# Kernel optimization log

Hardware: AMD Instinct MI355X
Metric: run time of the kernel (lower is better)

Reference implementation:

```python
import jax, jax.numpy as jnp
import numpy as np

HEADS = 16
EPS = 1e-5

def _ln(x, g, b):
    m = jnp.mean(x, axis=-1, keepdims=True)
    v = jnp.mean((x - m) ** 2, axis=-1, keepdims=True)
    return (x - m) * jax.lax.rsqrt(v + EPS) * g + b

def setup_inputs() -> dict:
    key = jax.random.key(0)
    ks = jax.random.split(key, 12)
    B, N, C, H = 4, 2048, 1024, 4096
    d = {}
    d['x'] = jax.random.normal(ks[0], (B, N, C), jnp.float32)
    d['pos_embed'] = jax.random.normal(ks[1], (1, N, C), jnp.float32)
    # LayerNorm params (normq, normk, normv, norm)
    for nm in ['nq', 'nk', 'nv', 'n']:
        d[nm + '_g'] = jnp.ones((C,), jnp.float32)
        d[nm + '_b'] = jnp.zeros((C,), jnp.float32)
    s = 1.0 / np.sqrt(C)
    d['wq'] = jax.random.uniform(ks[2], (C, C), jnp.float32, -s, s)
    d['bq'] = jnp.zeros((C,), jnp.float32)
    d['wk'] = jax.random.uniform(ks[3], (C, C), jnp.float32, -s, s)
    d['bk'] = jnp.zeros((C,), jnp.float32)
    d['wv'] = jax.random.uniform(ks[4], (C, C), jnp.float32, -s, s)
    d['bv'] = jnp.zeros((C,), jnp.float32)
    d['wp'] = jax.random.uniform(ks[5], (C, C), jnp.float32, -s, s)
    d['bp'] = jnp.zeros((C,), jnp.float32)
    d['w1'] = jax.random.uniform(ks[6], (C, H), jnp.float32, -s, s)
    d['b1'] = jnp.zeros((H,), jnp.float32)
    sh = 1.0 / np.sqrt(H)
    d['w2'] = jax.random.uniform(ks[7], (H, C), jnp.float32, -sh, sh)
    d['b2'] = jnp.zeros((C,), jnp.float32)
    return d

def reference(x, pos_embed, nq_g, nq_b, nk_g, nk_b, nv_g, nv_b, wq, bq, wk, bk, wv, bv, wp, bp, n_g, n_b, w1, b1, w2, b2):
    B, N, C = x.shape
    hd = C // HEADS
    scale = hd ** -0.5
    q_in = x
    k_in = x + pos_embed
    v_in = x + pos_embed
    # Attention (eval mode: dropout = identity)
    q = (_ln(q_in, nq_g, nq_b) @ wq + bq).reshape(B, N, HEADS, hd)
    k = (_ln(k_in, nk_g, nk_b) @ wk + bk).reshape(B, N, HEADS, hd)
    v = (_ln(v_in, nv_g, nv_b) @ wv + bv).reshape(B, N, HEADS, hd)
    attn = jnp.einsum('bqhd,bkhd->bhqk', q, k) * scale
    attn = jax.nn.softmax(attn, axis=-1)
    out = jnp.einsum('bhqk,bkhd->bqhd', attn, v).reshape(B, N, C)
    out = out @ wp + bp
    # residual + MLP
    h = q_in + out
    y = _ln(h, n_g, n_b) @ w1 + b1
    y = jnp.where(y >= 0, y, 0.1 * y)  # LeakyReLU(0.1)
    y = y @ w2 + b2
    return h + y
```

## Files before the change

kernel.cpp:

```cpp
#include <hip/hip_runtime.h>
#include <hip/hip_bf16.h>

#define DEV __device__ __forceinline__

typedef __attribute__((ext_vector_type(8))) short short8;
typedef __attribute__((ext_vector_type(4))) short short4v;
typedef __attribute__((ext_vector_type(4))) float f32x4;
typedef __attribute__((ext_vector_type(2))) int int2v;

constexpr int Bb   = 4;
constexpr int SEQ  = 2048;
constexpr int C    = 1024;
constexpr int HID  = 4096;
constexpr int NH   = 16;
constexpr int HD   = 64;
constexpr int MTOT = Bb * SEQ;

DEV unsigned bfbits(float f) {
  unsigned x = __float_as_uint(f);
  return (x + 0x7fffu + ((x >> 16) & 1u)) >> 16;
}

DEV short f2bf(float f) { return (short)bfbits(f); }

DEV unsigned packrn(float a, float b) {
  unsigned ua = __float_as_uint(a) + 0x8000u;
  unsigned ub = __float_as_uint(b) + 0x8000u;
  return __builtin_amdgcn_perm(ub, ua, 0x07060302u);
}

DEV float fexp2(float x) {
#if __has_builtin(__builtin_amdgcn_exp2f)
  return __builtin_amdgcn_exp2f(x);
#else
  float r;
  asm("v_exp_f32 %0, %1" : "=v"(r) : "v"(x));
  return r;
#endif
}

DEV void gload16(const void* g, void* l) {
  __builtin_amdgcn_global_load_lds((const __attribute__((address_space(1))) void*)g,
                                   (__attribute__((address_space(3))) void*)l, 16, 0, 0);
}

DEV f32x4 mfma16(short4v a, short4v b, f32x4 c) {
#if __has_builtin(__builtin_amdgcn_mfma_f32_16x16x16bf16_1k)
  return __builtin_amdgcn_mfma_f32_16x16x16bf16_1k(a, b, c, 0, 0, 0);
#else
  asm volatile("v_mfma_f32_16x16x16_bf16 %0, %1, %2, %0" : "+v"(c) : "v"(a), "v"(b));
  return c;
#endif
}

DEV void transpose_body(const float* __restrict__ src, short* __restrict__ dst,
                        int R, int Cc) {
  __shared__ float t[32][33];
  int tx = threadIdx.x & 31, ty = threadIdx.x >> 5;
  int c0 = blockIdx.x * 32, r0 = blockIdx.y * 32;
  #pragma unroll
  for (int i = 0; i < 4; i++)
    t[ty + i * 8][tx] = src[(size_t)(r0 + ty + i * 8) * Cc + c0 + tx];
  __syncthreads();
  #pragma unroll
  for (int i = 0; i < 4; i++)
    dst[(size_t)(c0 + ty + i * 8) * R + r0 + tx] = f2bf(t[tx][ty + i * 8]);
}

__global__ void k_transpose_w(const float* __restrict__ src, short* __restrict__ dst,
                              int R, int Cc) {
  transpose_body(src, dst, R, Cc);
}

__global__ void k_transpose_w4(const float* __restrict__ s0, const float* __restrict__ s1,
                               const float* __restrict__ s2, const float* __restrict__ s3,
                               short* __restrict__ d0, short* __restrict__ d1,
                               short* __restrict__ d2, short* __restrict__ d3) {
  const float* s = blockIdx.z == 0 ? s0 : blockIdx.z == 1 ? s1 : blockIdx.z == 2 ? s2 : s3;
  short*       d = blockIdx.z == 0 ? d0 : blockIdx.z == 1 ? d1 : blockIdx.z == 2 ? d2 : d3;
  transpose_body(s, d, C, C);
}

__global__ void k_transpose_v(const short* __restrict__ V, short* __restrict__ Vt) {
  __shared__ short t[32][33];
  int tx = threadIdx.x & 31, ty = threadIdx.x >> 5;
  int plane = blockIdx.z;
  int b = plane >> 4, h = plane & 15;
  int n0 = blockIdx.x * 32, d0 = blockIdx.y * 32;
  #pragma unroll
  for (int i = 0; i < 4; i++)
    t[ty + i * 8][tx] = V[(size_t)(b * SEQ + n0 + ty + i * 8) * C + h * HD + d0 + tx];
  __syncthreads();
  #pragma unroll
  for (int i = 0; i < 4; i++)
    Vt[((size_t)plane * HD + d0 + ty + i * 8) * SEQ + n0 + tx] = t[tx][ty + i * 8];
}

__global__ void k_ln_qkv(const float* __restrict__ x, const float* __restrict__ pos,
                         const float* __restrict__ nqg, const float* __restrict__ nqb,
                         const float* __restrict__ nkg, const float* __restrict__ nkb,
                         const float* __restrict__ nvg, const float* __restrict__ nvb,
                         short* __restrict__ xq, short* __restrict__ xk,
                         short* __restrict__ xv) {
  int row = blockIdx.x, tid = threadIdx.x;
  int n = row & (SEQ - 1);
  float a4[4], p4[4];
  float s1 = 0, s2 = 0, t1 = 0, t2 = 0;
  #pragma unroll
  for (int i = 0; i < 4; i++) {
    int c = tid + i * 256;
    float a = x[(size_t)row * C + c];
    float p = pos[(size_t)n * C + c] + a;
    a4[i] = a; p4[i] = p;
    s1 += a; s2 += a * a; t1 += p; t2 += p * p;
  }
  #pragma unroll
  for (int off = 32; off; off >>= 1) {
    s1 += __shfl_xor(s1, off, 64);
    s2 += __shfl_xor(s2, off, 64);
    t1 += __shfl_xor(t1, off, 64);
    t2 += __shfl_xor(t2, off, 64);
  }
  __shared__ float red[4][4];
  int wave = tid >> 6, lane = tid & 63;
  if (lane == 0) { red[wave][0] = s1; red[wave][1] = s2; red[wave][2] = t1; red[wave][3] = t2; }
  __syncthreads();
  s1 = red[0][0] + red[1][0] + red[2][0] + red[3][0];
  s2 = red[0][1] + red[1][1] + red[2][1] + red[3][1];
  t1 = red[0][2] + red[1][2] + red[2][2] + red[3][2];
  t2 = red[0][3] + red[1][3] + red[2][3] + red[3][3];
  float mq = s1 * (1.f / C), mk = t1 * (1.f / C);
  float rq = rsqrtf(s2 * (1.f / C) - mq * mq + 1e-5f);
  float rk = rsqrtf(t2 * (1.f / C) - mk * mk + 1e-5f);
  #pragma unroll
  for (int i = 0; i < 4; i++) {
    int c = tid + i * 256;
    float nq_ = (a4[i] - mq) * rq;
    float nk_ = (p4[i] - mk) * rk;
    xq[(size_t)row * C + c] = f2bf(nq_ * nqg[c] + nqb[c]);
    xk[(size_t)row * C + c] = f2bf(nk_ * nkg[c] + nkb[c]);
    xv[(size_t)row * C + c] = f2bf(nk_ * nvg[c] + nvb[c]);
  }
}

__global__ void k_ln1(const float* __restrict__ h, const float* __restrict__ g,
                      const float* __restrict__ bta, short* __restrict__ out) {
  int row = blockIdx.x, tid = threadIdx.x;
  float a4[4];
  float s1 = 0, s2 = 0;
  #pragma unroll
  for (int i = 0; i < 4; i++) {
    int c = tid + i * 256;
    float a = h[(size_t)row * C + c];
    a4[i] = a; s1 += a; s2 += a * a;
  }
  #pragma unroll
  for (int off = 32; off; off >>= 1) {
    s1 += __shfl_xor(s1, off, 64);
    s2 += __shfl_xor(s2, off, 64);
  }
  __shared__ float red[4][2];
  int wave = tid >> 6, lane = tid & 63;
  if (lane == 0) { red[wave][0] = s1; red[wave][1] = s2; }
  __syncthreads();
  s1 = red[0][0] + red[1][0] + red[2][0] + red[3][0];
  s2 = red[0][1] + red[1][1] + red[2][1] + red[3][1];
  float m = s1 * (1.f / C);
  float r = rsqrtf(s2 * (1.f / C) - m * m + 1e-5f);
  #pragma unroll
  for (int i = 0; i < 4; i++) {
    int c = tid + i * 256;
    out[(size_t)row * C + c] = f2bf((a4[i] - m) * r * g[c] + bta[c]);
  }
}

template <int MODE>
DEV void gemm8_body(const short* __restrict__ A, const short* __restrict__ Bt,
                    const float* __restrict__ bias, const float* __restrict__ resid,
                    void* __restrict__ outp, int Nn, int Kk, float scale,
                    int m0, int n0, short* __restrict__ sA, short* __restrict__ sB) {
  constexpr int AO = 128 * 64, BO = 256 * 64;
  const int tid = threadIdx.x;
  const int wave = tid >> 6, lane = tid & 63, quad = lane >> 4, l15 = lane & 15;
  const int wm = (wave >> 2) * 64, wn = (wave & 3) * 64;

  const int sr = tid >> 3, su = tid & 7;
  const int sx = (su ^ (sr & 7)) * 8;
  const short* gA0 = A + (size_t)(m0 + sr) * Kk + sx;
  const short* gA1 = gA0 + (size_t)64 * Kk;
  const short* gB0 = Bt + (size_t)(n0 + sr) * Kk + sx;
  const short* gB1 = gB0 + (size_t)64 * Kk;
  const short* gB2 = gB0 + (size_t)128 * Kk;
  const short* gB3 = gB0 + (size_t)192 * Kk;

  const f32x4 fzero = {0.f, 0.f, 0.f, 0.f};
  f32x4 acc[4][4];
  #pragma unroll
  for (int mi = 0; mi < 4; mi++)
    #pragma unroll
    for (int ni = 0; ni < 4; ni++) acc[mi][ni] = fzero;

  const int nkt = Kk >> 6;

  auto stg = [&](int t) {
    const int b_ = t % 3, ko = t << 6;
    gload16(gA0 + ko, &sA[(size_t)b_ * AO + (size_t)tid * 8]);
    gload16(gA1 + ko, &sA[(size_t)b_ * AO + (size_t)(512 + tid) * 8]);
    gload16(gB0 + ko, &sB[(size_t)b_ * BO + (size_t)tid * 8]);
    gload16(gB1 + ko, &sB[(size_t)b_ * BO + (size_t)(512 + tid) * 8]);
    gload16(gB2 + ko, &sB[(size_t)b_ * BO + (size_t)(1024 + tid) * 8]);
    gload16(gB3 + ko, &sB[(size_t)b_ * BO + (size_t)(1536 + tid) * 8]);
  };
  auto stgA_ = [&](int t) {
    const int b_ = t % 3, ko = t << 6;
    gload16(gA0 + ko, &sA[(size_t)b_ * AO + (size_t)tid * 8]);
    gload16(gA1 + ko, &sA[(size_t)b_ * AO + (size_t)(512 + tid) * 8]);
    gload16(gB0 + ko, &sB[(size_t)b_ * BO + (size_t)tid * 8]);
  };
  auto stgB_ = [&](int t) {
    const int b_ = t % 3, ko = t << 6;
    gload16(gB1 + ko, &sB[(size_t)b_ * BO + (size_t)(512 + tid) * 8]);
    gload16(gB2 + ko, &sB[(size_t)b_ * BO + (size_t)(1024 + tid) * 8]);
    gload16(gB3 + ko, &sB[(size_t)b_ * BO + (size_t)(1536 + tid) * 8]);
  };

  stg(0);
  if (nkt > 1) stg(1);

  for (int t = 0; t < nkt; t++) {
    if (t + 1 < nkt) asm volatile("s_waitcnt vmcnt(6)" ::: "memory");
    else             asm volatile("s_waitcnt vmcnt(0)" ::: "memory");
    __builtin_amdgcn_s_barrier();
    const short* a_ = &sA[(size_t)(t % 3) * AO];
    const short* b_ = &sB[(size_t)(t % 3) * BO];
    short8 av[4][2];
    {
      short8 bv[2][2];
      #pragma unroll
      for (int m2 = 0; m2 < 4; m2++) {
        const int rA = wm + m2 * 16 + l15, sw = rA & 7;
        #pragma unroll
        for (int ks = 0; ks < 2; ks++)
          av[m2][ks] = *(const short8*)&a_[rA * 64 + ((ks * 4 + quad) ^ sw) * 8];
      }
      #pragma unroll
      for (int n2 = 0; n2 < 2; n2++) {
        const int rB = wn + n2 * 16 + l15, sw = rB & 7;
        #pragma unroll
        for (int ks = 0; ks < 2; ks++)
          bv[n2][ks] = *(const short8*)&b_[rB * 64 + ((ks * 4 + quad) ^ sw) * 8];
      }
      if (t + 2 < nkt) stgA_(t + 2);
      __builtin_amdgcn_s_barrier();
      asm volatile("s_waitcnt lgkmcnt(0)" ::: "memory");
      __builtin_amdgcn_sched_barrier(0);
      __builtin_amdgcn_s_setprio(1);
      #pragma unroll
      for (int ks = 0; ks < 2; ks++)
        #pragma unroll
        for (int m2 = 0; m2 < 4; m2++)
          #pragma unroll
          for (int n2 = 0; n2 < 2; n2++)
            acc[m2][n2] = __builtin_amdgcn_mfma_f32_16x16x32_bf16(
                av[m2][ks], bv[n2][ks], acc[m2][n2], 0, 0, 0);
      __builtin_amdgcn_s_setprio(0);
      __builtin_amdgcn_s_barrier();
    }
    {
      short8 bv[2][2];
      #pragma unroll
      for (int n2 = 0; n2 < 2; n2++) {
        const int rB = wn + (2 + n2) * 16 + l15, sw = rB & 7;
        #pragma unroll
        for (int ks = 0; ks < 2; ks++)
          bv[n2][ks] = *(const short8*)&b_[rB * 64 + ((ks * 4 + quad) ^ sw) * 8];
      }
      if (t + 2 < nkt) stgB_(t + 2);
      __builtin_amdgcn_s_barrier();
      asm volatile("s_waitcnt lgkmcnt(0)" ::: "memory");
      __builtin_amdgcn_sched_barrier(0);
      __builtin_amdgcn_s_setprio(1);
      #pragma unroll
      for (int ks = 0; ks < 2; ks++)
        #pragma unroll
        for (int m2 = 0; m2 < 4; m2++)
          #pragma unroll
          for (int n2 = 0; n2 < 2; n2++)
            acc[m2][2 + n2] = __builtin_amdgcn_mfma_f32_16x16x32_bf16(
                av[m2][ks], bv[n2][ks], acc[m2][2 + n2], 0, 0, 0);
      __builtin_amdgcn_s_setprio(0);
      __builtin_amdgcn_s_barrier();
    }
  }

  float bb[4];
  #pragma unroll
  for (int ni = 0; ni < 4; ni++) bb[ni] = bias[n0 + wn + ni * 16 + l15];
  #pragma unroll
  for (int mi = 0; mi < 4; mi++) {
    #pragma unroll
    for (int ni = 0; ni < 4; ni++) {
      #pragma unroll
      for (int r = 0; r < 4; r++) {
        int row = m0 + wm + mi * 16 + quad * 4 + r;
        int col = n0 + wn + ni * 16 + l15;
        float v = (acc[mi][ni][r] + bb[ni]) * scale;
        if constexpr (MODE == 1) v = v >= 0.f ? v : 0.1f * v;
        if constexpr (MODE == 2)
          ((float*)outp)[(size_t)row * Nn + col] = resid[(size_t)row * Nn + col] + v;
        else
          ((short*)outp)[(size_t)row * Nn + col] = f2bf(v);
      }
    }
  }
}

template <int MODE>
__global__ __launch_bounds__(512, 1)
void k_gemm8(const short* __restrict__ A, const short* __restrict__ Bt,
             const float* __restrict__ bias, const float* __restrict__ resid,
             void* __restrict__ outp, int Nn, int Kk) {
  __shared__ __align__(16) short sA[3 * 128 * 64];
  __shared__ __align__(16) short sB[3 * 256 * 64];
  gemm8_body<MODE>(A, Bt, bias, resid, outp, Nn, Kk, 1.0f,
                   blockIdx.x * 128, blockIdx.y * 256, sA, sB);
}

template <int MODE>
DEV void gemm2_body(const short* __restrict__ A, const short* __restrict__ Bt,
                    const float* __restrict__ bias, const float* __restrict__ resid,
                    void* __restrict__ outp, int Nn, int Kk, float scale,
                    int m0, int n0, short* __restrict__ sA, short* __restrict__ sB) {
  constexpr int TO = 256 * 64;
  const int tid = threadIdx.x;
  const int wave = tid >> 6, lane = tid & 63, quad = lane >> 4, l15 = lane & 15;
  const int wm = (wave >> 2) * 128, wn = (wave & 3) * 64;

  const int sr = tid >> 3, su = tid & 7;
  const int sx = (su ^ (sr & 7)) * 8;
  const short* gA0 = A + (size_t)(m0 + sr) * Kk + sx;
  const short* gB0 = Bt + (size_t)(n0 + sr) * Kk + sx;

  const f32x4 fzero = {0.f, 0.f, 0.f, 0.f};
  f32x4 acc[8][4];
  #pragma unroll
  for (int mi = 0; mi < 8; mi++)
    #pragma unroll
    for (int ni = 0; ni < 4; ni++) acc[mi][ni] = fzero;

  const int nkt = Kk >> 6;

  auto stgPair = [&](int t, int p) {
    const int b_ = t & 1, ko = t << 6;
    gload16(gA0 + (size_t)(p * 64) * Kk + ko,
            &sA[(size_t)b_ * TO + (size_t)p * 4096 + (size_t)tid * 8]);
    gload16(gB0 + (size_t)(p * 64) * Kk + ko,
            &sB[(size_t)b_ * TO + (size_t)p * 4096 + (size_t)tid * 8]);
  };

  #pragma unroll
  for (int p = 0; p < 4; p++) stgPair(0, p);

  for (int t = 0; t < nkt; t++) {
    asm volatile("s_waitcnt vmcnt(0)" ::: "memory");
    __builtin_amdgcn_s_barrier();
    const short* a_ = &sA[(size_t)(t & 1) * TO];
    const short* b_ = &sB[(size_t)(t & 1) * TO];
    short8 bv[4][2];
    #pragma unroll
    for (int ph = 0; ph < 4; ph++) {
      short8 av[2][2];
      #pragma unroll
      for (int m2 = 0; m2 < 2; m2++) {
        const int rA = wm + (ph * 2 + m2) * 16 + l15, sw = rA & 7;
        #pragma unroll
        for (int ks = 0; ks < 2; ks++)
          av[m2][ks] = *(const short8*)&a_[rA * 64 + ((ks * 4 + quad) ^ sw) * 8];
      }
      if (ph == 0) {
        #pragma unroll
        for (int n2 = 0; n2 < 4; n2++) {
          const int rB = wn + n2 * 16 + l15, sw = rB & 7;
          #pragma unroll
          for (int ks = 0; ks < 2; ks++)
            bv[n2][ks] = *(const short8*)&b_[rB * 64 + ((ks * 4 + quad) ^ sw) * 8];
        }
      }
      if (t + 1 < nkt) stgPair(t + 1, ph);
      __builtin_amdgcn_s_barrier();
      asm volatile("s_waitcnt lgkmcnt(0)" ::: "memory");
      __builtin_amdgcn_sched_barrier(0);
      __builtin_amdgcn_s_setprio(1);
      #pragma unroll
      for (int ks = 0; ks < 2; ks++)
        #pragma unroll
        for (int m2 = 0; m2 < 2; m2++)
          #pragma unroll
          for (int n2 = 0; n2 < 4; n2++)
            acc[ph * 2 + m2][n2] = __builtin_amdgcn_mfma_f32_16x16x32_bf16(
                av[m2][ks], bv[n2][ks], acc[ph * 2 + m2][n2], 0, 0, 0);
      __builtin_amdgcn_s_setprio(0);
      __builtin_amdgcn_s_barrier();
    }
  }

  float bb[4];
  #pragma unroll
  for (int ni = 0; ni < 4; ni++) bb[ni] = bias[n0 + wn + ni * 16 + l15];
  #pragma unroll
  for (int mi = 0; mi < 8; mi++) {
    #pragma unroll
    for (int ni = 0; ni < 4; ni++) {
      #pragma unroll
      for (int r = 0; r < 4; r++) {
        int row = m0 + wm + mi * 16 + quad * 4 + r;
        int col = n0 + wn + ni * 16 + l15;
        float v = (acc[mi][ni][r] + bb[ni]) * scale;
        if constexpr (MODE == 1) v = v >= 0.f ? v : 0.1f * v;
        if constexpr (MODE == 2)
          ((float*)outp)[(size_t)row * Nn + col] = resid[(size_t)row * Nn + col] + v;
        else
          ((short*)outp)[(size_t)row * Nn + col] = f2bf(v);
      }
    }
  }
}

template <int MODE>
__global__ __launch_bounds__(512, 1)
void k_gemm2(const short* __restrict__ A, const short* __restrict__ Bt,
             const float* __restrict__ bias, const float* __restrict__ resid,
             void* __restrict__ outp, int Nn, int Kk) {
  __shared__ __align__(16) short sA[2 * 256 * 64];
  __shared__ __align__(16) short sB[2 * 256 * 64];
  gemm2_body<MODE>(A, Bt, bias, resid, outp, Nn, Kk, 1.0f,
                   blockIdx.x * 256, blockIdx.y * 256, sA, sB);
}

__global__ __launch_bounds__(512, 1)
void k_gemm2_qkv(const short* __restrict__ xq, const short* __restrict__ xk,
                 const short* __restrict__ xv,
                 const short* __restrict__ wqT, const short* __restrict__ wkT,
                 const short* __restrict__ wvT,
                 const float* __restrict__ bq, const float* __restrict__ bk,
                 const float* __restrict__ bv,
                 short* __restrict__ Qm, short* __restrict__ Km, short* __restrict__ Vm) {
  __shared__ __align__(16) short sA[2 * 256 * 64];
  __shared__ __align__(16) short sB[2 * 256 * 64];
  const int z = blockIdx.z;
  const short* A    = z == 0 ? xq : z == 1 ? xk : xv;
  const short* Bt   = z == 0 ? wqT : z == 1 ? wkT : wvT;
  const float* bias = z == 0 ? bq : z == 1 ? bk : bv;
  short* outp       = z == 0 ? Qm : z == 1 ? Km : Vm;
  const float scale = z == 0 ? 0.1803368801111244f : 1.0f;
  gemm2_body<0>(A, Bt, bias, nullptr, outp, C, C, scale,
                blockIdx.x * 256, blockIdx.y * 256, sA, sB);
}

__global__ __launch_bounds__(256, 4)
void k_attn(const short* __restrict__ Q, const short* __restrict__ K,
            const short* __restrict__ Vt, short* __restrict__ O) {
  __shared__ __align__(16) short sK[2][64 * 64];
  __shared__ __align__(16) short sV[2][64 * 64];
  const int tid = threadIdx.x;
  const int bh = blockIdx.x;
  const int b = bh >> 4, h = bh & 15;
  const int q0 = blockIdx.y * 128;
  const int wave = tid >> 6, lane = tid & 63, quad = lane >> 4, l15 = lane & 15;
  const int wm = wave * 32;
  const size_t tokBase = (size_t)b * SEQ;

  short8 qf[2][2];
  #pragma unroll
  for (int qi = 0; qi < 2; qi++)
    #pragma unroll
    for (int hf = 0; hf < 2; hf++)
      qf[qi][hf] = *(const short8*)(Q + (tokBase + q0 + wm + qi * 16 + l15) * C
                                    + h * HD + hf * 32 + quad * 8);

  const int r0 = tid >> 3,        c0s = ((tid & 7) ^ (r0 & 7)) * 8;
  const int r1 = (tid + 256) >> 3, c1s = ((tid & 7) ^ (r1 & 7)) * 8;
  const short* gK0 = K + (tokBase + r0) * C + h * HD + c0s;
  const short* gK1 = K + (tokBase + r1) * C + h * HD + c1s;
  const short* gV0 = Vt + ((size_t)bh * HD + r0) * SEQ + c0s;
  const short* gV1 = Vt + ((size_t)bh * HD + r1) * SEQ + c1s;
  short* lK0 = &sK[0][tid * 8];
  short* lK1 = &sK[0][(tid + 256) * 8];
  short* lV0 = &sV[0][tid * 8];
  short* lV1 = &sV[0][(tid + 256) * 8];
  constexpr int BUFO = 64 * 64;

#define STAGE(bufsel, kb) {                                   \
    int kk = (kb) * 64, bo = (bufsel) * BUFO;                 \
    gload16(gK0 + (size_t)kk * C, lK0 + bo);                  \
    gload16(gK1 + (size_t)kk * C, lK1 + bo);                  \
    gload16(gV0 + kk,             lV0 + bo);                  \
    gload16(gV1 + kk,             lV1 + bo); }

  const f32x4 fzero = {0.f, 0.f, 0.f, 0.f};
  const short4v onesv = {0x3F80, 0x3F80, 0x3F80, 0x3F80};
  f32x4 o[2][4];
  f32x4 oSum[2] = {fzero, fzero};
  #pragma unroll
  for (int qi = 0; qi < 2; qi++)
    #pragma unroll
    for (int di = 0; di < 4; di++) o[qi][di] = fzero;

  const int sw = l15 & 7;

  STAGE(0, 0)

  for (int kb = 0; kb < SEQ / 64; kb++) {
    const int buf = kb & 1;
    __syncthreads();
    if (kb + 1 < SEQ / 64) STAGE(buf ^ 1, kb + 1)

    unsigned pk[4][2][2];
    #pragma unroll
    for (int ki = 0; ki < 4; ki++) {
      const int krow = (ki * 16 + l15) * 64;
      short8 a0 = *(const short8*)&sK[buf][krow + ((0 + quad) ^ sw) * 8];
      short8 a1 = *(const short8*)&sK[buf][krow + ((4 + quad) ^ sw) * 8];
      #pragma unroll
      for (int qi = 0; qi < 2; qi++) {
        f32x4 st = __builtin_amdgcn_mfma_f32_16x16x32_bf16(a0, qf[qi][0], fzero, 0, 0, 0);
        st = __builtin_amdgcn_mfma_f32_16x16x32_bf16(a1, qf[qi][1], st, 0, 0, 0);
        float p0 = fexp2(st[0]), p1 = fexp2(st[1]);
        float p2 = fexp2(st[2]), p3 = fexp2(st[3]);
        pk[ki][qi][0] = packrn(p0, p1);
        pk[ki][qi][1] = packrn(p2, p3);
      }
    }

    #pragma unroll
    for (int ki = 0; ki < 4; ki++) {
      short4v bv[4];
      const int g = ((ki * 2 + (quad >> 1)) ^ sw) * 8 + (quad & 1) * 4;
      #pragma unroll
      for (int di = 0; di < 4; di++)
        bv[di] = *(const short4v*)&sV[buf][(di * 16 + l15) * 64 + g];
      #pragma unroll
      for (int qi = 0; qi < 2; qi++) {
        int2v t; t.x = (int)pk[ki][qi][0]; t.y = (int)pk[ki][qi][1];
        short4v aP = __builtin_bit_cast(short4v, t);
        oSum[qi] = mfma16(aP, onesv, oSum[qi]);
        #pragma unroll
        for (int di = 0; di < 4; di++)
          o[qi][di] = mfma16(aP, bv[di], o[qi][di]);
      }
    }
  }
#undef STAGE

  float linv[2][4];
  #pragma unroll
  for (int qi = 0; qi < 2; qi++)
    #pragma unroll
    for (int r = 0; r < 4; r++)
      linv[qi][r] = 1.0f / oSum[qi][r];

  #pragma unroll
  for (int qi = 0; qi < 2; qi++)
    #pragma unroll
    for (int di = 0; di < 4; di++)
      #pragma unroll
      for (int r = 0; r < 4; r++) {
        int row = q0 + wm + qi * 16 + quad * 4 + r;
        int col = h * HD + di * 16 + l15;
        O[(tokBase + row) * C + col] = f2bf(o[qi][di][r] * linv[qi][r]);
      }
}

extern "C" void kernel_launch(void* const* d_in, const int* in_sizes, int n_in,
                              void* d_out, int out_size, void* d_ws, size_t ws_size,
                              hipStream_t stream) {
  const float* x   = (const float*)d_in[0];
  const float* pos = (const float*)d_in[1];
  const float* nqg = (const float*)d_in[2];
  const float* nqb = (const float*)d_in[3];
  const float* nkg = (const float*)d_in[4];
  const float* nkb = (const float*)d_in[5];
  const float* nvg = (const float*)d_in[6];
  const float* nvb = (const float*)d_in[7];
  const float* ng  = (const float*)d_in[8];
  const float* nb  = (const float*)d_in[9];
  const float* wq  = (const float*)d_in[10];
  const float* bq  = (const float*)d_in[11];
  const float* wk  = (const float*)d_in[12];
  const float* bk  = (const float*)d_in[13];
  const float* wv  = (const float*)d_in[14];
  const float* bv  = (const float*)d_in[15];
  const float* wp  = (const float*)d_in[16];
  const float* bp  = (const float*)d_in[17];
  const float* w1  = (const float*)d_in[18];
  const float* b1  = (const float*)d_in[19];
  const float* w2  = (const float*)d_in[20];
  const float* b2  = (const float*)d_in[21];

  char* ws = (char*)d_ws;
  const size_t MB = 1u << 20;
  short* wqT  = (short*)(ws + 0 * MB);
  short* wkT  = (short*)(ws + 2 * MB);
  short* wvT  = (short*)(ws + 4 * MB);
  short* wpT  = (short*)(ws + 6 * MB);
  short* w1T  = (short*)(ws + 8 * MB);
  short* w2T  = (short*)(ws + 16 * MB);
  short* xq   = (short*)(ws + 24 * MB);
  short* xk   = (short*)(ws + 40 * MB);
  short* xv   = (short*)(ws + 56 * MB);
  short* Qm   = (short*)(ws + 72 * MB);
  short* Km   = (short*)(ws + 88 * MB);
  short* Vm   = (short*)(ws + 104 * MB);
  short* Vt   = (short*)(ws + 120 * MB);
  short* y1   = (short*)(ws + 72 * MB);
  short* Ob   = xk;
  short* hln  = xq;
  float* hbuf = (float*)(ws + 136 * MB);
  (void)ws_size; (void)in_sizes; (void)n_in; (void)out_size;

  dim3 blk(256);
  k_transpose_w4<<<dim3(32, 32, 4), blk, 0, stream>>>(wq, wk, wv, wp, wqT, wkT, wvT, wpT);
  k_transpose_w<<<dim3(128, 32), blk, 0, stream>>>(w1, w1T, C, HID);
  k_transpose_w<<<dim3(32, 128), blk, 0, stream>>>(w2, w2T, HID, C);
  k_ln_qkv<<<dim3(MTOT), blk, 0, stream>>>(x, pos, nqg, nqb, nkg, nkb, nvg, nvb, xq, xk, xv);
  k_gemm2_qkv<<<dim3(MTOT / 256, C / 256, 3), dim3(512), 0, stream>>>(
      xq, xk, xv, wqT, wkT, wvT, bq, bk, bv, Qm, Km, Vm);
  k_transpose_v<<<dim3(SEQ / 32, HD / 32, Bb * NH), blk, 0, stream>>>(Vm, Vt);
  k_attn<<<dim3(Bb * NH, SEQ / 128), blk, 0, stream>>>(Qm, Km, Vt, Ob);
  k_gemm8<2><<<dim3(MTOT / 128, C / 256), dim3(512), 0, stream>>>(Ob, wpT, bp, x, hbuf, C, C);
  k_ln1<<<dim3(MTOT), blk, 0, stream>>>(hbuf, ng, nb, hln);
  k_gemm2<1><<<dim3(MTOT / 256, HID / 256), dim3(512), 0, stream>>>(hln, w1T, b1, nullptr,
                                                                    y1, HID, C);
  k_gemm8<2><<<dim3(MTOT / 128, C / 256), dim3(512), 0, stream>>>(y1, w2T, b2, hbuf,
                                                                  (float*)d_out, C, HID);
}
```

Baseline: 518.7 us.

## Split attention block across 8 waves with 16 query rows each, add setprio

The attention kernel now launches 512 threads per block, so each of 8 waves owns 16 query rows instead of 4 waves owning 32. The K/V tile staging is spread across twice as many threads, and s_setprio is placed around the MFMA sequences. The aim is more waves in flight to hide LDS and exp latency and more even MFMA issue. In exchange, each loaded K/V fragment is reused by fewer MFMAs per wave, so LDS read traffic rises, and the 8-block occupancy bound may limit registers.

```diff
diff --git a/kernel.cpp b/kernel.cpp
--- a/kernel.cpp
+++ b/kernel.cpp
@@ -457,7 +457,7 @@
                 blockIdx.x * 256, blockIdx.y * 256, sA, sB);
 }
 
-__global__ __launch_bounds__(256, 4)
+__global__ __launch_bounds__(512, 8)
 void k_attn(const short* __restrict__ Q, const short* __restrict__ K,
             const short* __restrict__ Vt, short* __restrict__ O) {
   __shared__ __align__(16) short sK[2][64 * 64];
@@ -467,44 +467,33 @@
   const int b = bh >> 4, h = bh & 15;
   const int q0 = blockIdx.y * 128;
   const int wave = tid >> 6, lane = tid & 63, quad = lane >> 4, l15 = lane & 15;
-  const int wm = wave * 32;
+  const int wm = wave * 16;
   const size_t tokBase = (size_t)b * SEQ;
 
-  short8 qf[2][2];
-  #pragma unroll
-  for (int qi = 0; qi < 2; qi++)
-    #pragma unroll
-    for (int hf = 0; hf < 2; hf++)
-      qf[qi][hf] = *(const short8*)(Q + (tokBase + q0 + wm + qi * 16 + l15) * C
-                                    + h * HD + hf * 32 + quad * 8);
-
-  const int r0 = tid >> 3,        c0s = ((tid & 7) ^ (r0 & 7)) * 8;
-  const int r1 = (tid + 256) >> 3, c1s = ((tid & 7) ^ (r1 & 7)) * 8;
+  short8 qf[2];
+  #pragma unroll
+  for (int hf = 0; hf < 2; hf++)
+    qf[hf] = *(const short8*)(Q + (tokBase + q0 + wm + l15) * C
+                              + h * HD + hf * 32 + quad * 8);
+
+  const int r0 = tid >> 3, c0s = ((tid & 7) ^ (r0 & 7)) * 8;
   const short* gK0 = K + (tokBase + r0) * C + h * HD + c0s;
-  const short* gK1 = K + (tokBase + r1) * C + h * HD + c1s;
   const short* gV0 = Vt + ((size_t)bh * HD + r0) * SEQ + c0s;
-  const short* gV1 = Vt + ((size_t)bh * HD + r1) * SEQ + c1s;
   short* lK0 = &sK[0][tid * 8];
-  short* lK1 = &sK[0][(tid + 256) * 8];
   short* lV0 = &sV[0][tid * 8];
-  short* lV1 = &sV[0][(tid + 256) * 8];
   constexpr int BUFO = 64 * 64;
 
 #define STAGE(bufsel, kb) {                                   \
     int kk = (kb) * 64, bo = (bufsel) * BUFO;                 \
     gload16(gK0 + (size_t)kk * C, lK0 + bo);                  \
-    gload16(gK1 + (size_t)kk * C, lK1 + bo);                  \
-    gload16(gV0 + kk,             lV0 + bo);                  \
-    gload16(gV1 + kk,             lV1 + bo); }
+    gload16(gV0 + kk,             lV0 + bo); }
 
   const f32x4 fzero = {0.f, 0.f, 0.f, 0.f};
   const short4v onesv = {0x3F80, 0x3F80, 0x3F80, 0x3F80};
-  f32x4 o[2][4];
-  f32x4 oSum[2] = {fzero, fzero};
-  #pragma unroll
-  for (int qi = 0; qi < 2; qi++)
-    #pragma unroll
-    for (int di = 0; di < 4; di++) o[qi][di] = fzero;
+  f32x4 o[4];
+  f32x4 oSum = fzero;
+  #pragma unroll
+  for (int di = 0; di < 4; di++) o[di] = fzero;
 
   const int sw = l15 & 7;
 
@@ -515,21 +504,20 @@
     __syncthreads();
     if (kb + 1 < SEQ / 64) STAGE(buf ^ 1, kb + 1)
 
-    unsigned pk[4][2][2];
+    unsigned pk[4][2];
     #pragma unroll
     for (int ki = 0; ki < 4; ki++) {
       const int krow = (ki * 16 + l15) * 64;
       short8 a0 = *(const short8*)&sK[buf][krow + ((0 + quad) ^ sw) * 8];
       short8 a1 = *(const short8*)&sK[buf][krow + ((4 + quad) ^ sw) * 8];
-      #pragma unroll
-      for (int qi = 0; qi < 2; qi++) {
-        f32x4 st = __builtin_amdgcn_mfma_f32_16x16x32_bf16(a0, qf[qi][0], fzero, 0, 0, 0);
-        st = __builtin_amdgcn_mfma_f32_16x16x32_bf16(a1, qf[qi][1], st, 0, 0, 0);
-        float p0 = fexp2(st[0]), p1 = fexp2(st[1]);
-        float p2 = fexp2(st[2]), p3 = fexp2(st[3]);
-        pk[ki][qi][0] = packrn(p0, p1);
-        pk[ki][qi][1] = packrn(p2, p3);
-      }
+      __builtin_amdgcn_s_setprio(1);
+      f32x4 st = __builtin_amdgcn_mfma_f32_16x16x32_bf16(a0, qf[0], fzero, 0, 0, 0);
+      st = __builtin_amdgcn_mfma_f32_16x16x32_bf16(a1, qf[1], st, 0, 0, 0);
+      __builtin_amdgcn_s_setprio(0);
+      float p0 = fexp2(st[0]), p1 = fexp2(st[1]);
+      float p2 = fexp2(st[2]), p3 = fexp2(st[3]);
+      pk[ki][0] = packrn(p0, p1);
+      pk[ki][1] = packrn(p2, p3);
     }
 
     #pragma unroll
@@ -539,36 +527,31 @@
       #pragma unroll
       for (int di = 0; di < 4; di++)
         bv[di] = *(const short4v*)&sV[buf][(di * 16 + l15) * 64 + g];
-      #pragma unroll
-      for (int qi = 0; qi < 2; qi++) {
-        int2v t; t.x = (int)pk[ki][qi][0]; t.y = (int)pk[ki][qi][1];
-        short4v aP = __builtin_bit_cast(short4v, t);
-        oSum[qi] = mfma16(aP, onesv, oSum[qi]);
-        #pragma unroll
-        for (int di = 0; di < 4; di++)
-          o[qi][di] = mfma16(aP, bv[di], o[qi][di]);
-      }
+      int2v t; t.x = (int)pk[ki][0]; t.y = (int)pk[ki][1];
+      short4v aP = __builtin_bit_cast(short4v, t);
+      __builtin_amdgcn_s_setprio(1);
+      oSum = mfma16(aP, onesv, oSum);
+      #pragma unroll
+      for (int di = 0; di < 4; di++)
+        o[di] = mfma16(aP, bv[di], o[di]);
+      __builtin_amdgcn_s_setprio(0);
     }
   }
 #undef STAGE
 
-  float linv[2][4];
-  #pragma unroll
-  for (int qi = 0; qi < 2; qi++)
-    #pragma unroll
-    for (int r = 0; r < 4; r++)
-      linv[qi][r] = 1.0f / oSum[qi][r];
-
-  #pragma unroll
-  for (int qi = 0; qi < 2; qi++)
-    #pragma unroll
-    for (int di = 0; di < 4; di++)
-      #pragma unroll
-      for (int r = 0; r < 4; r++) {
-        int row = q0 + wm + qi * 16 + quad * 4 + r;
-        int col = h * HD + di * 16 + l15;
-        O[(tokBase + row) * C + col] = f2bf(o[qi][di][r] * linv[qi][r]);
-      }
+  float linv[4];
+  #pragma unroll
+  for (int r = 0; r < 4; r++)
+    linv[r] = 1.0f / oSum[r];
+
+  #pragma unroll
+  for (int di = 0; di < 4; di++)
+    #pragma unroll
+    for (int r = 0; r < 4; r++) {
+      int row = q0 + wm + quad * 4 + r;
+      int col = h * HD + di * 16 + l15;
+      O[(tokBase + row) * C + col] = f2bf(o[di][r] * linv[r]);
+    }
 }
 
 extern "C" void kernel_launch(void* const* d_in, const int* in_sizes, int n_in,
@@ -626,7 +609,7 @@
   k_gemm2_qkv<<<dim3(MTOT / 256, C / 256, 3), dim3(512), 0, stream>>>(
       xq, xk, xv, wqT, wkT, wvT, bq, bk, bv, Qm, Km, Vm);
   k_transpose_v<<<dim3(SEQ / 32, HD / 32, Bb * NH), blk, 0, stream>>>(Vm, Vt);
-  k_attn<<<dim3(Bb * NH, SEQ / 128), blk, 0, stream>>>(Qm, Km, Vt, Ob);
+  k_attn<<<dim3(Bb * NH, SEQ / 128), dim3(512), 0, stream>>>(Qm, Km, Vt, Ob);
   k_gemm8<2><<<dim3(MTOT / 128, C / 256), dim3(512), 0, stream>>>(Ob, wpT, bp, x, hbuf, C, C);
   k_ln1<<<dim3(MTOT), blk, 0, stream>>>(hbuf, ng, nb, hln);
   k_gemm2<1><<<dim3(MTOT / 256, HID / 256), dim3(512), 0, stream>>>(hln, w1T, b1, nullptr,
```

After: 542.9 us. 4.7% more time.
